# Kernel tuning notes

Hardware: AMD Instinct MI355X
Metric: run time of the kernel (lower is better)

## Reference

```python
import jax, jax.numpy as jnp
import numpy as np

IOU_THRESHOLD = 0.5
NEGATIVE_RATIO = 3
ALPHA = 1.0
B, A, D, G = 64, 8732, 85, 32  # batch, anchors, 4+81 classes, max gt per image


def cxcywh_to_xyxy(b):
    cx, cy, w, h = b[..., 0], b[..., 1], b[..., 2], b[..., 3]
    return jnp.stack([cx - w / 2, cy - h / 2, cx + w / 2, cy + h / 2], axis=-1)


def box_iou(a, b):
    # a: (G,4) xyxy, b: (A,4) xyxy -> (G,A)
    lt = jnp.maximum(a[:, None, :2], b[None, :, :2])
    rb = jnp.minimum(a[:, None, 2:], b[None, :, 2:])
    wh = jnp.clip(rb - lt, 0.0)
    inter = wh[..., 0] * wh[..., 1]
    area_a = (a[:, 2] - a[:, 0]) * (a[:, 3] - a[:, 1])
    area_b = (b[:, 2] - b[:, 0]) * (b[:, 3] - b[:, 1])
    return inter / (area_a[:, None] + area_b[None, :] - inter)


def encode(gt, anchors):
    g_cxcy = (gt[:, :2] - anchors[:, :2]) / anchors[:, 2:]
    g_wh = jnp.log(gt[:, 2:]) - jnp.log(anchors[:, 2:])
    return jnp.concatenate([g_cxcy, g_wh], axis=-1)


def match_one(gt_box, gt_label, count, anchors):
    # gt_box (G,4) cxcywh, gt_label (G,), count scalar, anchors (A,4) cxcywh
    num_anchors = anchors.shape[0]
    valid = jnp.arange(gt_box.shape[0]) < count
    iou = box_iou(cxcywh_to_xyxy(gt_box), cxcywh_to_xyxy(anchors))  # (G,A)
    iou = jnp.where(valid[:, None], iou, -1.0)
    best_gt_overlap = iou.max(0)
    best_gt_idx = iou.argmax(0)
    over = best_gt_overlap > IOU_THRESHOLD
    loc = jnp.where(over[:, None], encode(gt_box[best_gt_idx], anchors), 0.0)
    cls = jnp.where(over, gt_label[best_gt_idx].astype(jnp.float32) + 1.0, 0.0)
    # force-match: each (valid) gt claims its best anchor, overwriting
    best_prior_idx = iou.argmax(1)  # (G,)
    idx = jnp.where(valid, best_prior_idx, num_anchors)  # dump invalid gt into a scratch row
    loc = jnp.concatenate([loc, jnp.zeros((1, 4), loc.dtype)], 0)
    loc = loc.at[idx].set(encode(gt_box, anchors[best_prior_idx]))[:num_anchors]
    cls = jnp.concatenate([cls, jnp.zeros((1,), cls.dtype)], 0)
    cls = cls.at[idx].set(gt_label.astype(jnp.float32) + 1.0)[:num_anchors]
    return loc, cls


def smooth_l1(d):
    ad = jnp.abs(d)
    return jnp.where(ad < 1.0, 0.5 * d * d, ad - 0.5)


def multibox_loss(pred, anchors, gt_boxes, gt_labels, gt_counts):
    num_anchors = pred.shape[1]
    loc_pred, conf_pred = pred[:, :, :4], pred[:, :, 4:]
    target_loc, target_cls = jax.vmap(match_one, in_axes=(0, 0, 0, None))(
        gt_boxes, gt_labels, gt_counts, anchors)  # (B,A,4), (B,A)
    pos = target_cls > 0  # (B,A)
    posf = pos.astype(pred.dtype)
    n_pos = posf.sum(1)  # (B,) guaranteed > 0 since every image has >=1 gt
    # localization: per-element smooth-L1 on positives, normalized per image
    loc_l = smooth_l1(loc_pred - target_loc) * posf[:, :, None]
    loc_loss = jnp.sum(loc_l / n_pos[:, None, None])
    # classification CE per anchor
    logp = jax.nn.log_softmax(conf_pred, axis=-1)  # (B,A,C)
    cls_ce = -jnp.take_along_axis(logp, target_cls.astype(jnp.int32)[:, :, None], axis=-1)[..., 0]
    pos_loss = jnp.sum(cls_ce * posf / n_pos[:, None])
    # hard negative mining (double-sort rank trick, no grad through selection)
    num_neg = jnp.minimum(NEGATIVE_RATIO * pos.sum(1), num_anchors - 1)  # (B,) int
    all_neg = jax.lax.stop_gradient(jnp.where(pos, 0.0, cls_ce))
    order = jnp.argsort(-all_neg, axis=1)
    rank = jnp.argsort(order, axis=1)
    neg_mask = (rank < num_neg[:, None]).astype(pred.dtype)
    neg_ce = -logp[:, :, 0]  # CE against background class 0
    neg_loss = jnp.sum(neg_ce * neg_mask / n_pos[:, None])
    return ALPHA * loc_loss + pos_loss + neg_loss


def setup_inputs() -> dict:
    key = jax.random.key(0)
    k1, k2, k3, k4, k5, k6, k7 = jax.random.split(key, 7)
    pred = jax.random.normal(k1, (B, A, D), dtype=jnp.float32)
    anchors = jnp.concatenate([
        jax.random.uniform(k2, (A, 2), minval=0.0, maxval=1.0),
        jax.random.uniform(k3, (A, 2), minval=0.05, maxval=0.5)], axis=-1)
    gt_boxes = jnp.concatenate([
        jax.random.uniform(k4, (B, G, 2), minval=0.0, maxval=1.0),
        jax.random.uniform(k5, (B, G, 2), minval=0.05, maxval=0.6)], axis=-1)
    gt_labels = jax.random.randint(k6, (B, G), 0, 80)
    gt_counts = jax.random.randint(k7, (B,), 1, G + 1)
    return {"pred": pred, "anchors": anchors, "gt_boxes": gt_boxes,
            "gt_labels": gt_labels, "gt_counts": gt_counts}


def reference(pred, anchors, gt_boxes, gt_labels, gt_counts):
    return multibox_loss(pred, anchors, gt_boxes, gt_labels, gt_counts)
```

## Files before the change

### kernel.cpp

```cpp
#include <hip/hip_runtime.h>
#include <math.h>

#define BB 64
#define AA 8732
#define DD 85
#define GG 32
#define CC 81
#define TILE 64
#define RPB 4
#define NTB 35
#define NAB 35


typedef __attribute__((address_space(3))) unsigned int lds_u32;
typedef const __attribute__((address_space(1))) unsigned int glb_u32;

__device__ __forceinline__ float smoothl1(float d) {
  float ad = fabsf(d);
  return ad < 1.0f ? 0.5f * d * d : ad - 0.5f;
}

__device__ __forceinline__ float frcp(float x) {
  return __builtin_amdgcn_rcpf(x);
}

__global__ __launch_bounds__(256) void k_match(
    const float* __restrict__ anchors, const float* __restrict__ gt_boxes,
    const int* __restrict__ gt_counts, int* __restrict__ match,
    int* __restrict__ bestp, int* __restrict__ n_pos, int* __restrict__ done_sel)
{
  const int b = blockIdx.y;
  const int count = gt_counts[b];
  __shared__ float gx0[GG], gy0[GG], gx1[GG], gy1[GG], gar[GG];
  __shared__ float wv[4];
  __shared__ int wi[4];

  if (blockIdx.x < NAB) {
    if (blockIdx.x == 0 && threadIdx.x == 0) {
      n_pos[b] = 0;
      if (b == 0) *done_sel = 0;
    }
    if (threadIdx.x < GG) {
      float4 gb = reinterpret_cast<const float4*>(gt_boxes)[b * GG + threadIdx.x];
      float x0 = gb.x - gb.z * 0.5f, y0 = gb.y - gb.w * 0.5f;
      float x1 = gb.x + gb.z * 0.5f, y1 = gb.y + gb.w * 0.5f;
      gx0[threadIdx.x] = x0; gy0[threadIdx.x] = y0;
      gx1[threadIdx.x] = x1; gy1[threadIdx.x] = y1;
      gar[threadIdx.x] = (x1 - x0) * (y1 - y0);
    }
    __syncthreads();
    const int a = blockIdx.x * 256 + threadIdx.x;
    if (a < AA) {
      float4 an = reinterpret_cast<const float4*>(anchors)[a];
      float ax0 = an.x - an.z * 0.5f, ay0 = an.y - an.w * 0.5f;
      float ax1 = an.x + an.z * 0.5f, ay1 = an.y + an.w * 0.5f;
      float aar = (ax1 - ax0) * (ay1 - ay0);
      float best = -1.0f; int bi = 0;
      for (int g = 0; g < count; ++g) {
        float iw = fmaxf(fminf(gx1[g], ax1) - fmaxf(gx0[g], ax0), 0.0f);
        float ih = fmaxf(fminf(gy1[g], ay1) - fmaxf(gy0[g], ay0), 0.0f);
        float inter = iw * ih;
        float iou = inter * frcp(gar[g] + aar - inter);
        if (iou > best) { best = iou; bi = g; }
      }
      match[b * AA + a] = (best > 0.5f) ? bi : -1;
    }
  } else {
    const int g = blockIdx.x - NAB;
    if (g < count) {
      float4 gb = reinterpret_cast<const float4*>(gt_boxes)[b * GG + g];
      const float gx0s = gb.x - gb.z * 0.5f, gy0s = gb.y - gb.w * 0.5f;
      const float gx1s = gb.x + gb.z * 0.5f, gy1s = gb.y + gb.w * 0.5f;
      const float gars = (gx1s - gx0s) * (gy1s - gy0s);

      float bv = -2.0f; int bi = AA;
      for (int a = threadIdx.x; a < AA; a += 256) {
        float4 an = reinterpret_cast<const float4*>(anchors)[a];
        float ax0 = an.x - an.z * 0.5f, ay0 = an.y - an.w * 0.5f;
        float ax1 = an.x + an.z * 0.5f, ay1 = an.y + an.w * 0.5f;
        float aar = (ax1 - ax0) * (ay1 - ay0);
        float iw = fmaxf(fminf(gx1s, ax1) - fmaxf(gx0s, ax0), 0.0f);
        float ih = fmaxf(fminf(gy1s, ay1) - fmaxf(gy0s, ay0), 0.0f);
        float inter = iw * ih;
        float iou = inter * frcp(gars + aar - inter);
        if (iou > bv || (iou == bv && a < bi)) { bv = iou; bi = a; }
      }
      #pragma unroll
      for (int m = 1; m < 64; m <<= 1) {
        float ov = __shfl_xor(bv, m);
        int   oi = __shfl_xor(bi, m);
        if (ov > bv || (ov == bv && oi < bi)) { bv = ov; bi = oi; }
      }
      if ((threadIdx.x & 63) == 0) { wv[threadIdx.x >> 6] = bv; wi[threadIdx.x >> 6] = bi; }
      __syncthreads();
      if (threadIdx.x == 0) {
        float fv = wv[0]; int fi = wi[0];
        #pragma unroll
        for (int w = 1; w < 4; ++w)
          if (wv[w] > fv || (wv[w] == fv && wi[w] < fi)) { fv = wv[w]; fi = wi[w]; }
        bestp[b * GG + g] = fi;
      }
    }
  }
}

__global__ __launch_bounds__(256) void k_loss(
    const float* __restrict__ pred, const float* __restrict__ anchors,
    const float* __restrict__ gt_boxes, const int* __restrict__ gt_labels,
    const int* __restrict__ gt_counts, const int* __restrict__ match,
    const int* __restrict__ bestp, float* __restrict__ all_neg,
    float* __restrict__ partials, int* __restrict__ n_pos)
{
  const int b = blockIdx.y;
  const int abase = blockIdx.x * RPB * TILE;
  const int tid = threadIdx.x;
  __shared__ int ovr[RPB * TILE];
  __shared__ float4 sgb[GG];
  __shared__ int slab[GG];
  __shared__ float wsum[4];
  __shared__ int wcnt[4];

  const int cnt = gt_counts[b];
  if (tid < GG) {
    sgb[tid] = reinterpret_cast<const float4*>(gt_boxes)[b * GG + tid];
    slab[tid] = gt_labels[b * GG + tid];
  }
  ovr[tid] = -1;
  __syncthreads();
  if (tid < GG && tid < cnt) {
    int p = bestp[b * GG + tid];
    int rel = p - abase;
    if (rel >= 0 && rel < RPB * TILE) atomicMax(&ovr[rel], tid);
  }
  __syncthreads();

  const int r = tid >> 2;
  const int sub = tid & 3;
  float acc = 0.0f;
  int poscnt = 0;

  for (int i = 0; i < RPB; ++i) {
    const int a0 = abase + i * TILE;
    if (a0 >= AA) break;
    const int a = a0 + r;
    if (a < AA) {
      const float* base = pred + ((size_t)b * AA + a) * DD;
      float4 s0 = *(const float4*)(base + (sub)      * 4);
      float4 s1 = *(const float4*)(base + (sub + 4)  * 4);
      float4 s2 = *(const float4*)(base + (sub + 8)  * 4);
      float4 s3 = *(const float4*)(base + (sub + 12) * 4);
      float4 s4 = *(const float4*)(base + (sub + 16) * 4);
      float4 s5f = make_float4(0.f, 0.f, 0.f, 0.f);
      float  s5x = 0.0f;
      if (sub == 0) s5f = *(const float4*)(base + 80);
      if (sub == 1) s5x = base[84];

      int m = match[b * AA + a];
      { int o = ovr[a - abase]; if (o >= 0) m = o; }
      const int tgt = (m >= 0) ? slab[m] + 1 : 0;

      const int cb = 4 * sub - 4;
      float mx = -INFINITY, xt = -INFINITY;
      #define SCAN(v, ccb)                                                   \
        { mx = fmaxf(fmaxf(fmaxf(mx, (v).x), (v).y), fmaxf((v).z, (v).w));   \
          if ((ccb) + 0 == tgt) xt = (v).x;                                  \
          if ((ccb) + 1 == tgt) xt = (v).y;                                  \
          if ((ccb) + 2 == tgt) xt = (v).z;                                  \
          if ((ccb) + 3 == tgt) xt = (v).w; }
      if (sub > 0) SCAN(s0, cb);
      SCAN(s1, cb + 16); SCAN(s2, cb + 32); SCAN(s3, cb + 48); SCAN(s4, cb + 64);
      if (sub == 0) SCAN(s5f, 76);
      if (sub == 1) { mx = fmaxf(mx, s5x); if (tgt == 80) xt = s5x; }
      #undef SCAN
      #pragma unroll
      for (int msk = 1; msk <= 2; msk <<= 1)
        mx = fmaxf(mx, __shfl_xor(mx, msk));

      float s = 0.0f;
      #define ESUM(v) s += __expf((v).x - mx) + __expf((v).y - mx) +          \
                           __expf((v).z - mx) + __expf((v).w - mx);
      if (sub > 0) ESUM(s0);
      ESUM(s1); ESUM(s2); ESUM(s3); ESUM(s4);
      if (sub == 0) ESUM(s5f);
      if (sub == 1) s += __expf(s5x - mx);
      #undef ESUM
      #pragma unroll
      for (int msk = 1; msk <= 2; msk <<= 1) {
        s  += __shfl_xor(s, msk);
        xt  = fmaxf(xt, __shfl_xor(xt, msk));
      }
      const float lse = mx + __logf(s);
      const float ce = lse - xt;

      if (sub == 0) {
        if (m >= 0) {
          poscnt += 1;
          float4 an = reinterpret_cast<const float4*>(anchors)[a];
          float4 gb = sgb[m];
          float tx = (gb.x - an.x) / an.z;
          float ty = (gb.y - an.y) / an.w;
          float tw = __logf(gb.z) - __logf(an.z);
          float th = __logf(gb.w) - __logf(an.w);
          acc += smoothl1(s0.x - tx) + smoothl1(s0.y - ty)
               + smoothl1(s0.z - tw) + smoothl1(s0.w - th) + ce;
          all_neg[b * AA + a] = 0.0f;
        } else {
          all_neg[b * AA + a] = fmaxf(ce, 0.0f);
        }
      }
    }
  }

  #pragma unroll
  for (int msk = 1; msk < 64; msk <<= 1) {
    acc    += __shfl_xor(acc, msk);
    poscnt += __shfl_xor(poscnt, msk);
  }
  if ((tid & 63) == 0) {
    wsum[tid >> 6] = acc;
    wcnt[tid >> 6] = poscnt;
  }
  __syncthreads();
  if (tid == 0) {
    partials[b * NTB + blockIdx.x] = (wsum[0] + wsum[1]) + (wsum[2] + wsum[3]);
    int c = wcnt[0] + wcnt[1] + wcnt[2] + wcnt[3];
    if (c) atomicAdd(&n_pos[b], c);
  }
}

__global__ __launch_bounds__(1024) void k_select(
    const float* __restrict__ all_neg, const float* __restrict__ partials,
    const int* __restrict__ n_pos, float* __restrict__ batch_total,
    int* __restrict__ done_sel, float* __restrict__ out)
{
  const int b = blockIdx.x;
  const int tid = threadIdx.x;
  __shared__ unsigned u[AA];
  __shared__ int hist16[16][257];
  __shared__ int hist[256];
  __shared__ unsigned sh_pref;
  __shared__ int sh_k;
  __shared__ int sflag;
  __shared__ float wf[16];
  __shared__ int wc[16];

  {
    const float* srcg = all_neg + (size_t)b * AA;
    #pragma unroll
    for (int j = 0; j < 3; ++j) {
      int c = j * 1024 + tid;
      if (c < 2183)
        __builtin_amdgcn_global_load_lds(
            (glb_u32*)(srcg + c * 4), (lds_u32*)((float*)u + c * 4), 16, 0, 0);
    }
  }

  float ps = 0.0f;
  if (tid < 64) {
    float pv = (tid < NTB) ? partials[b * NTB + tid] : 0.0f;
    #pragma unroll
    for (int m = 1; m < 64; m <<= 1) pv += __shfl_xor(pv, m);
    ps = pv;
  }
  __syncthreads();

  const int np = n_pos[b];
  const int K = min(3 * np, AA - 1);
  const int wvid = tid >> 6;

  unsigned prefix = 0;
  int kk = K;
  for (int shift = 24; shift >= 0; shift -= 8) {
    int* hflat = &hist16[0][0];
    for (int i = tid; i < 16 * 257; i += 1024) hflat[i] = 0;
    __syncthreads();
    const unsigned hmask = (shift == 24) ? 0u : (0xFFFFFFFFu << (shift + 8));
    for (int i = tid; i < AA; i += 1024) {
      unsigned x = u[i];
      if ((x & hmask) == prefix)
        atomicAdd(&hist16[wvid][(x >> shift) & 255], 1);
    }
    __syncthreads();
    if (tid < 256) {
      int s = 0;
      #pragma unroll
      for (int h = 0; h < 16; ++h) s += hist16[h][tid];
      hist[tid] = s;
    }
    __syncthreads();
    if (tid < 64) {
      int h0 = hist[4 * tid], h1 = hist[4 * tid + 1];
      int h2 = hist[4 * tid + 2], h3 = hist[4 * tid + 3];
      int lsum = h0 + h1 + h2 + h3;
      int suf = lsum;
      #pragma unroll
      for (int off = 1; off < 64; off <<= 1) {
        int o = __shfl_down(suf, off);
        suf += (tid + off < 64) ? o : 0;
      }
      int after = suf - lsum;
      int s3 = h3 + after, s2 = h2 + s3, s1 = h1 + s2, s0 = h0 + s1;
      if (s0 >= kk && s1 < kk)    { sh_pref = prefix | ((unsigned)(4*tid+0) << shift); sh_k = kk - s1; }
      if (s1 >= kk && s2 < kk)    { sh_pref = prefix | ((unsigned)(4*tid+1) << shift); sh_k = kk - s2; }
      if (s2 >= kk && s3 < kk)    { sh_pref = prefix | ((unsigned)(4*tid+2) << shift); sh_k = kk - s3; }
      if (s3 >= kk && after < kk) { sh_pref = prefix | ((unsigned)(4*tid+3) << shift); sh_k = kk - after; }
    }
    __syncthreads();
    prefix = sh_pref;
    kk = sh_k;
    __syncthreads();
  }
  const float tstar = __uint_as_float(prefix);

  float ssum = 0.0f; int cgt = 0;
  for (int i = tid; i < AA; i += 1024) {
    float x = __uint_as_float(u[i]);
    if (x > tstar) { ssum += x; cgt += 1; }
  }
  #pragma unroll
  for (int m = 1; m < 64; m <<= 1) {
    ssum += __shfl_xor(ssum, m);
    cgt  += __shfl_xor(cgt, m);
  }
  if ((tid & 63) == 0) { wf[wvid] = ssum; wc[wvid] = cgt; }
  __syncthreads();
  if (tid == 0) {
    float S = 0.0f; int Cg = 0;
    #pragma unroll
    for (int w = 0; w < 16; ++w) { S += wf[w]; Cg += wc[w]; }
    float neg_sum = S + (float)(K - Cg) * tstar;
    batch_total[b] = (ps + neg_sum) / (float)np;
    __threadfence();
    int old = atomicAdd(done_sel, 1);
    sflag = (old == BB - 1) ? 1 : 0;
  }
  __syncthreads();

  if (sflag) {
    __threadfence();
    if (tid < 64) {
      float v = batch_total[tid];
      #pragma unroll
      for (int m = 1; m < 64; m <<= 1) v += __shfl_xor(v, m);
      if (tid == 0) out[0] = v;
    }
  }
}

extern "C" void kernel_launch(void* const* d_in, const int* in_sizes, int n_in,
                              void* d_out, int out_size, void* d_ws, size_t ws_size,
                              hipStream_t stream) {
  (void)in_sizes; (void)n_in; (void)out_size; (void)ws_size;
  const float* pred      = (const float*)d_in[0];
  const float* anchors   = (const float*)d_in[1];
  const float* gt_boxes  = (const float*)d_in[2];
  const int*   gt_labels = (const int*)d_in[3];
  const int*   gt_counts = (const int*)d_in[4];

  char* ws = (char*)d_ws;
  int*   match       = (int*)(ws + 0);
  float* all_neg     = (float*)(ws + 2235392);
  float* partials    = (float*)(ws + 4470784);
  float* batch_total = (float*)(ws + 4479744);
  int*   bestp       = (int*)(ws + 4480000);
  int*   n_pos       = (int*)(ws + 4488192);
  int*   done_sel    = (int*)(ws + 4488448);
  float* out = (float*)d_out;

  hipLaunchKernelGGL(k_match, dim3(NAB + GG, BB), dim3(256), 0, stream,
                     anchors, gt_boxes, gt_counts, match, bestp, n_pos, done_sel);
  hipLaunchKernelGGL(k_loss, dim3(NTB, BB), dim3(256), 0, stream,
                     pred, anchors, gt_boxes, gt_labels, gt_counts, match, bestp,
                     all_neg, partials, n_pos);
  hipLaunchKernelGGL(k_select, dim3(BB), dim3(1024), 0, stream,
                     all_neg, partials, n_pos, batch_total, done_sel, out);
}
```

Baseline: 85.41 us.

## Fuse matching into loss kernel and apply force-match corrections in select

New measurement: 89.84 us. 5.2% more time.

```diff
diff --git a/kernel.cpp b/kernel.cpp
--- a/kernel.cpp
+++ b/kernel.cpp
@@ -8,8 +8,8 @@
 #define CC 81
 #define TILE 64
 #define RPB 4
-#define NTB 35
-#define NAB 35
+#define NLB 35
+#define NSB GG
 
 
 typedef __attribute__((address_space(3))) unsigned int lds_u32;
@@ -24,222 +24,202 @@
   return __builtin_amdgcn_rcpf(x);
 }
 
-__global__ __launch_bounds__(256) void k_match(
-    const float* __restrict__ anchors, const float* __restrict__ gt_boxes,
-    const int* __restrict__ gt_counts, int* __restrict__ match,
-    int* __restrict__ bestp, int* __restrict__ n_pos, int* __restrict__ done_sel)
+__global__ __launch_bounds__(256) void k_fused(
+    const float* __restrict__ pred, const float* __restrict__ anchors,
+    const float* __restrict__ gt_boxes, const int* __restrict__ gt_labels,
+    const int* __restrict__ gt_counts, float* __restrict__ all_neg,
+    float* __restrict__ partials, int* __restrict__ poscnts,
+    int* __restrict__ bestp, unsigned* __restrict__ epoch)
 {
   const int b = blockIdx.y;
-  const int count = gt_counts[b];
-  __shared__ float gx0[GG], gy0[GG], gx1[GG], gy1[GG], gar[GG];
-  __shared__ float wv[4];
-  __shared__ int wi[4];
-
-  if (blockIdx.x < NAB) {
-    if (blockIdx.x == 0 && threadIdx.x == 0) {
-      n_pos[b] = 0;
-      if (b == 0) *done_sel = 0;
-    }
-    if (threadIdx.x < GG) {
-      float4 gb = reinterpret_cast<const float4*>(gt_boxes)[b * GG + threadIdx.x];
+  const int tid = threadIdx.x;
+  const int cnt = gt_counts[b];
+
+  __shared__ float sgx0[GG], sgy0[GG], sgx1[GG], sgy1[GG], sgar[GG];
+  __shared__ float4 sgb[GG];
+  __shared__ int slab[GG];
+  __shared__ float wsum[4];
+  __shared__ int wcnt[4];
+
+  if (blockIdx.x < NLB) {
+    if (blockIdx.x == 0 && b == 0 && tid == 0) *epoch = 0u;
+    if (tid < GG) {
+      float4 gb = reinterpret_cast<const float4*>(gt_boxes)[b * GG + tid];
+      sgb[tid] = gb;
       float x0 = gb.x - gb.z * 0.5f, y0 = gb.y - gb.w * 0.5f;
       float x1 = gb.x + gb.z * 0.5f, y1 = gb.y + gb.w * 0.5f;
-      gx0[threadIdx.x] = x0; gy0[threadIdx.x] = y0;
-      gx1[threadIdx.x] = x1; gy1[threadIdx.x] = y1;
-      gar[threadIdx.x] = (x1 - x0) * (y1 - y0);
-    }
-    __syncthreads();
-    const int a = blockIdx.x * 256 + threadIdx.x;
-    if (a < AA) {
+      sgx0[tid] = x0; sgy0[tid] = y0; sgx1[tid] = x1; sgy1[tid] = y1;
+      sgar[tid] = (x1 - x0) * (y1 - y0);
+      slab[tid] = gt_labels[b * GG + tid];
+    }
+    __syncthreads();
+
+    const int abase = blockIdx.x * RPB * TILE;
+    const int r = tid >> 2;
+    const int sub = tid & 3;
+    float acc = 0.0f;
+    int poscnt = 0;
+
+    for (int i = 0; i < RPB; ++i) {
+      const int a0 = abase + i * TILE;
+      if (a0 >= AA) break;
+      const int a = a0 + r;
+      if (a < AA) {
+        const float* base = pred + ((size_t)b * AA + a) * DD;
+        float4 s0 = *(const float4*)(base + (sub)      * 4);
+        float4 s1 = *(const float4*)(base + (sub + 4)  * 4);
+        float4 s2 = *(const float4*)(base + (sub + 8)  * 4);
+        float4 s3 = *(const float4*)(base + (sub + 12) * 4);
+        float4 s4 = *(const float4*)(base + (sub + 16) * 4);
+        float4 s5f = make_float4(0.f, 0.f, 0.f, 0.f);
+        float  s5x = 0.0f;
+        if (sub == 0) s5f = *(const float4*)(base + 80);
+        if (sub == 1) s5x = base[84];
+        float4 an = reinterpret_cast<const float4*>(anchors)[a];
+
+        float ax0 = an.x - an.z * 0.5f, ay0 = an.y - an.w * 0.5f;
+        float ax1 = an.x + an.z * 0.5f, ay1 = an.y + an.w * 0.5f;
+        float aar = (ax1 - ax0) * (ay1 - ay0);
+        float bv = -1.0f; int bg = 0;
+        for (int g = sub; g < cnt; g += 4) {
+          float iw = fmaxf(fminf(sgx1[g], ax1) - fmaxf(sgx0[g], ax0), 0.0f);
+          float ih = fmaxf(fminf(sgy1[g], ay1) - fmaxf(sgy0[g], ay0), 0.0f);
+          float inter = iw * ih;
+          float iou = inter * frcp(sgar[g] + aar - inter);
+          if (iou > bv) { bv = iou; bg = g; }
+        }
+        #pragma unroll
+        for (int msk = 1; msk <= 2; msk <<= 1) {
+          float ov = __shfl_xor(bv, msk);
+          int   og = __shfl_xor(bg, msk);
+          if (ov > bv || (ov == bv && og < bg)) { bv = ov; bg = og; }
+        }
+        const int m = (bv > 0.5f) ? bg : -1;
+        const int tgt = (m >= 0) ? slab[m] + 1 : 0;
+
+        const int cb = 4 * sub - 4;
+        float mx = -INFINITY, xt = -INFINITY;
+        #define SCAN(v, ccb)                                                 \
+          { mx = fmaxf(fmaxf(fmaxf(mx, (v).x), (v).y), fmaxf((v).z, (v).w)); \
+            if ((ccb) + 0 == tgt) xt = (v).x;                                \
+            if ((ccb) + 1 == tgt) xt = (v).y;                                \
+            if ((ccb) + 2 == tgt) xt = (v).z;                                \
+            if ((ccb) + 3 == tgt) xt = (v).w; }
+        if (sub > 0) SCAN(s0, cb);
+        SCAN(s1, cb + 16); SCAN(s2, cb + 32); SCAN(s3, cb + 48); SCAN(s4, cb + 64);
+        if (sub == 0) SCAN(s5f, 76);
+        if (sub == 1) { mx = fmaxf(mx, s5x); if (tgt == 80) xt = s5x; }
+        #undef SCAN
+        #pragma unroll
+        for (int msk = 1; msk <= 2; msk <<= 1)
+          mx = fmaxf(mx, __shfl_xor(mx, msk));
+
+        float s = 0.0f;
+        #define ESUM(v) s += __expf((v).x - mx) + __expf((v).y - mx) +        \
+                             __expf((v).z - mx) + __expf((v).w - mx);
+        if (sub > 0) ESUM(s0);
+        ESUM(s1); ESUM(s2); ESUM(s3); ESUM(s4);
+        if (sub == 0) ESUM(s5f);
+        if (sub == 1) s += __expf(s5x - mx);
+        #undef ESUM
+        #pragma unroll
+        for (int msk = 1; msk <= 2; msk <<= 1) {
+          s  += __shfl_xor(s, msk);
+          xt  = fmaxf(xt, __shfl_xor(xt, msk));
+        }
+        const float lse = mx + __logf(s);
+        const float ce = lse - xt;
+
+        if (sub == 0) {
+          if (m >= 0) {
+            poscnt += 1;
+            float4 gb = sgb[m];
+            float tx = (gb.x - an.x) / an.z;
+            float ty = (gb.y - an.y) / an.w;
+            float tw = __logf(gb.z) - __logf(an.z);
+            float th = __logf(gb.w) - __logf(an.w);
+            acc += smoothl1(s0.x - tx) + smoothl1(s0.y - ty)
+                 + smoothl1(s0.z - tw) + smoothl1(s0.w - th) + ce;
+            all_neg[b * AA + a] = 0.0f;
+          } else {
+            all_neg[b * AA + a] = fmaxf(ce, 0.0f);
+          }
+        }
+      }
+    }
+
+    #pragma unroll
+    for (int msk = 1; msk < 64; msk <<= 1) {
+      acc    += __shfl_xor(acc, msk);
+      poscnt += __shfl_xor(poscnt, msk);
+    }
+    if ((tid & 63) == 0) { wsum[tid >> 6] = acc; wcnt[tid >> 6] = poscnt; }
+    __syncthreads();
+    if (tid == 0) {
+      partials[b * NLB + blockIdx.x] = (wsum[0] + wsum[1]) + (wsum[2] + wsum[3]);
+      poscnts[b * NLB + blockIdx.x] = wcnt[0] + wcnt[1] + wcnt[2] + wcnt[3];
+    }
+  } else {
+    const int g = blockIdx.x - NLB;
+    if (g >= cnt) return;
+
+    float4 gb = reinterpret_cast<const float4*>(gt_boxes)[b * GG + g];
+    const float gx0s = gb.x - gb.z * 0.5f, gy0s = gb.y - gb.w * 0.5f;
+    const float gx1s = gb.x + gb.z * 0.5f, gy1s = gb.y + gb.w * 0.5f;
+    const float gars = (gx1s - gx0s) * (gy1s - gy0s);
+
+    float bv = -2.0f; int bi = AA;
+    for (int a = tid; a < AA; a += 256) {
       float4 an = reinterpret_cast<const float4*>(anchors)[a];
       float ax0 = an.x - an.z * 0.5f, ay0 = an.y - an.w * 0.5f;
       float ax1 = an.x + an.z * 0.5f, ay1 = an.y + an.w * 0.5f;
       float aar = (ax1 - ax0) * (ay1 - ay0);
-      float best = -1.0f; int bi = 0;
-      for (int g = 0; g < count; ++g) {
-        float iw = fmaxf(fminf(gx1[g], ax1) - fmaxf(gx0[g], ax0), 0.0f);
-        float ih = fmaxf(fminf(gy1[g], ay1) - fmaxf(gy0[g], ay0), 0.0f);
-        float inter = iw * ih;
-        float iou = inter * frcp(gar[g] + aar - inter);
-        if (iou > best) { best = iou; bi = g; }
-      }
-      match[b * AA + a] = (best > 0.5f) ? bi : -1;
-    }
-  } else {
-    const int g = blockIdx.x - NAB;
-    if (g < count) {
-      float4 gb = reinterpret_cast<const float4*>(gt_boxes)[b * GG + g];
-      const float gx0s = gb.x - gb.z * 0.5f, gy0s = gb.y - gb.w * 0.5f;
-      const float gx1s = gb.x + gb.z * 0.5f, gy1s = gb.y + gb.w * 0.5f;
-      const float gars = (gx1s - gx0s) * (gy1s - gy0s);
-
-      float bv = -2.0f; int bi = AA;
-      for (int a = threadIdx.x; a < AA; a += 256) {
-        float4 an = reinterpret_cast<const float4*>(anchors)[a];
-        float ax0 = an.x - an.z * 0.5f, ay0 = an.y - an.w * 0.5f;
-        float ax1 = an.x + an.z * 0.5f, ay1 = an.y + an.w * 0.5f;
-        float aar = (ax1 - ax0) * (ay1 - ay0);
-        float iw = fmaxf(fminf(gx1s, ax1) - fmaxf(gx0s, ax0), 0.0f);
-        float ih = fmaxf(fminf(gy1s, ay1) - fmaxf(gy0s, ay0), 0.0f);
-        float inter = iw * ih;
-        float iou = inter * frcp(gars + aar - inter);
-        if (iou > bv || (iou == bv && a < bi)) { bv = iou; bi = a; }
-      }
+      float iw = fmaxf(fminf(gx1s, ax1) - fmaxf(gx0s, ax0), 0.0f);
+      float ih = fmaxf(fminf(gy1s, ay1) - fmaxf(gy0s, ay0), 0.0f);
+      float inter = iw * ih;
+      float iou = inter * frcp(gars + aar - inter);
+      if (iou > bv || (iou == bv && a < bi)) { bv = iou; bi = a; }
+    }
+    #pragma unroll
+    for (int m = 1; m < 64; m <<= 1) {
+      float ov = __shfl_xor(bv, m);
+      int   oi = __shfl_xor(bi, m);
+      if (ov > bv || (ov == bv && oi < bi)) { bv = ov; bi = oi; }
+    }
+    if ((tid & 63) == 0) { wsum[tid >> 6] = bv; wcnt[tid >> 6] = bi; }
+    __syncthreads();
+    if (tid == 0) {
+      float fv = wsum[0]; int fi = wcnt[0];
       #pragma unroll
-      for (int m = 1; m < 64; m <<= 1) {
-        float ov = __shfl_xor(bv, m);
-        int   oi = __shfl_xor(bi, m);
-        if (ov > bv || (ov == bv && oi < bi)) { bv = ov; bi = oi; }
-      }
-      if ((threadIdx.x & 63) == 0) { wv[threadIdx.x >> 6] = bv; wi[threadIdx.x >> 6] = bi; }
-      __syncthreads();
-      if (threadIdx.x == 0) {
-        float fv = wv[0]; int fi = wi[0];
-        #pragma unroll
-        for (int w = 1; w < 4; ++w)
-          if (wv[w] > fv || (wv[w] == fv && wi[w] < fi)) { fv = wv[w]; fi = wi[w]; }
-        bestp[b * GG + g] = fi;
-      }
+      for (int w = 1; w < 4; ++w)
+        if (wsum[w] > fv || (wsum[w] == fv && wcnt[w] < fi)) { fv = wsum[w]; fi = wcnt[w]; }
+      bestp[b * GG + g] = fi;
     }
   }
 }
 
-__global__ __launch_bounds__(256) void k_loss(
+__global__ __launch_bounds__(1024) void k_select(
     const float* __restrict__ pred, const float* __restrict__ anchors,
     const float* __restrict__ gt_boxes, const int* __restrict__ gt_labels,
-    const int* __restrict__ gt_counts, const int* __restrict__ match,
-    const int* __restrict__ bestp, float* __restrict__ all_neg,
-    float* __restrict__ partials, int* __restrict__ n_pos)
-{
-  const int b = blockIdx.y;
-  const int abase = blockIdx.x * RPB * TILE;
-  const int tid = threadIdx.x;
-  __shared__ int ovr[RPB * TILE];
-  __shared__ float4 sgb[GG];
-  __shared__ int slab[GG];
-  __shared__ float wsum[4];
-  __shared__ int wcnt[4];
-
-  const int cnt = gt_counts[b];
-  if (tid < GG) {
-    sgb[tid] = reinterpret_cast<const float4*>(gt_boxes)[b * GG + tid];
-    slab[tid] = gt_labels[b * GG + tid];
-  }
-  ovr[tid] = -1;
-  __syncthreads();
-  if (tid < GG && tid < cnt) {
-    int p = bestp[b * GG + tid];
-    int rel = p - abase;
-    if (rel >= 0 && rel < RPB * TILE) atomicMax(&ovr[rel], tid);
-  }
-  __syncthreads();
-
-  const int r = tid >> 2;
-  const int sub = tid & 3;
-  float acc = 0.0f;
-  int poscnt = 0;
-
-  for (int i = 0; i < RPB; ++i) {
-    const int a0 = abase + i * TILE;
-    if (a0 >= AA) break;
-    const int a = a0 + r;
-    if (a < AA) {
-      const float* base = pred + ((size_t)b * AA + a) * DD;
-      float4 s0 = *(const float4*)(base + (sub)      * 4);
-      float4 s1 = *(const float4*)(base + (sub + 4)  * 4);
-      float4 s2 = *(const float4*)(base + (sub + 8)  * 4);
-      float4 s3 = *(const float4*)(base + (sub + 12) * 4);
-      float4 s4 = *(const float4*)(base + (sub + 16) * 4);
-      float4 s5f = make_float4(0.f, 0.f, 0.f, 0.f);
-      float  s5x = 0.0f;
-      if (sub == 0) s5f = *(const float4*)(base + 80);
-      if (sub == 1) s5x = base[84];
-
-      int m = match[b * AA + a];
-      { int o = ovr[a - abase]; if (o >= 0) m = o; }
-      const int tgt = (m >= 0) ? slab[m] + 1 : 0;
-
-      const int cb = 4 * sub - 4;
-      float mx = -INFINITY, xt = -INFINITY;
-      #define SCAN(v, ccb)                                                   \
-        { mx = fmaxf(fmaxf(fmaxf(mx, (v).x), (v).y), fmaxf((v).z, (v).w));   \
-          if ((ccb) + 0 == tgt) xt = (v).x;                                  \
-          if ((ccb) + 1 == tgt) xt = (v).y;                                  \
-          if ((ccb) + 2 == tgt) xt = (v).z;                                  \
-          if ((ccb) + 3 == tgt) xt = (v).w; }
-      if (sub > 0) SCAN(s0, cb);
-      SCAN(s1, cb + 16); SCAN(s2, cb + 32); SCAN(s3, cb + 48); SCAN(s4, cb + 64);
-      if (sub == 0) SCAN(s5f, 76);
-      if (sub == 1) { mx = fmaxf(mx, s5x); if (tgt == 80) xt = s5x; }
-      #undef SCAN
-      #pragma unroll
-      for (int msk = 1; msk <= 2; msk <<= 1)
-        mx = fmaxf(mx, __shfl_xor(mx, msk));
-
-      float s = 0.0f;
-      #define ESUM(v) s += __expf((v).x - mx) + __expf((v).y - mx) +          \
-                           __expf((v).z - mx) + __expf((v).w - mx);
-      if (sub > 0) ESUM(s0);
-      ESUM(s1); ESUM(s2); ESUM(s3); ESUM(s4);
-      if (sub == 0) ESUM(s5f);
-      if (sub == 1) s += __expf(s5x - mx);
-      #undef ESUM
-      #pragma unroll
-      for (int msk = 1; msk <= 2; msk <<= 1) {
-        s  += __shfl_xor(s, msk);
-        xt  = fmaxf(xt, __shfl_xor(xt, msk));
-      }
-      const float lse = mx + __logf(s);
-      const float ce = lse - xt;
-
-      if (sub == 0) {
-        if (m >= 0) {
-          poscnt += 1;
-          float4 an = reinterpret_cast<const float4*>(anchors)[a];
-          float4 gb = sgb[m];
-          float tx = (gb.x - an.x) / an.z;
-          float ty = (gb.y - an.y) / an.w;
-          float tw = __logf(gb.z) - __logf(an.z);
-          float th = __logf(gb.w) - __logf(an.w);
-          acc += smoothl1(s0.x - tx) + smoothl1(s0.y - ty)
-               + smoothl1(s0.z - tw) + smoothl1(s0.w - th) + ce;
-          all_neg[b * AA + a] = 0.0f;
-        } else {
-          all_neg[b * AA + a] = fmaxf(ce, 0.0f);
-        }
-      }
-    }
-  }
-
-  #pragma unroll
-  for (int msk = 1; msk < 64; msk <<= 1) {
-    acc    += __shfl_xor(acc, msk);
-    poscnt += __shfl_xor(poscnt, msk);
-  }
-  if ((tid & 63) == 0) {
-    wsum[tid >> 6] = acc;
-    wcnt[tid >> 6] = poscnt;
-  }
-  __syncthreads();
-  if (tid == 0) {
-    partials[b * NTB + blockIdx.x] = (wsum[0] + wsum[1]) + (wsum[2] + wsum[3]);
-    int c = wcnt[0] + wcnt[1] + wcnt[2] + wcnt[3];
-    if (c) atomicAdd(&n_pos[b], c);
-  }
-}
-
-__global__ __launch_bounds__(1024) void k_select(
-    const float* __restrict__ all_neg, const float* __restrict__ partials,
-    const int* __restrict__ n_pos, float* __restrict__ batch_total,
-    int* __restrict__ done_sel, float* __restrict__ out)
+    const int* __restrict__ gt_counts, const float* __restrict__ all_neg,
+    const float* __restrict__ partials, const int* __restrict__ poscnts,
+    const int* __restrict__ bestp, float* __restrict__ batch_total,
+    unsigned* __restrict__ epoch, float* __restrict__ out)
 {
   const int b = blockIdx.x;
   const int tid = threadIdx.x;
   __shared__ unsigned u[AA];
   __shared__ int hist16[16][257];
   __shared__ int hist[256];
+  __shared__ float sgx0[GG], sgy0[GG], sgx1[GG], sgy1[GG], sgar[GG];
+  __shared__ float4 sgb[GG];
+  __shared__ int slab[GG];
+  __shared__ float sdelta[GG];
+  __shared__ int sdnp[GG];
   __shared__ unsigned sh_pref;
   __shared__ int sh_k;
+  __shared__ int sh_np;
+  __shared__ float sh_base;
   __shared__ int sflag;
   __shared__ float wf[16];
   __shared__ int wc[16];
@@ -254,22 +234,89 @@
             (glb_u32*)(srcg + c * 4), (lds_u32*)((float*)u + c * 4), 16, 0, 0);
     }
   }
-
-  float ps = 0.0f;
+  if (tid < GG) {
+    float4 gb = reinterpret_cast<const float4*>(gt_boxes)[b * GG + tid];
+    sgb[tid] = gb;
+    float x0 = gb.x - gb.z * 0.5f, y0 = gb.y - gb.w * 0.5f;
+    float x1 = gb.x + gb.z * 0.5f, y1 = gb.y + gb.w * 0.5f;
+    sgx0[tid] = x0; sgy0[tid] = y0; sgx1[tid] = x1; sgy1[tid] = y1;
+    sgar[tid] = (x1 - x0) * (y1 - y0);
+    slab[tid] = gt_labels[b * GG + tid];
+    sdelta[tid] = 0.0f; sdnp[tid] = 0;
+  }
+
+  float ps = 0.0f; int pc = 0;
   if (tid < 64) {
-    float pv = (tid < NTB) ? partials[b * NTB + tid] : 0.0f;
+    float pv = (tid < NLB) ? partials[b * NLB + tid] : 0.0f;
+    int   cv = (tid < NLB) ? poscnts[b * NLB + tid] : 0;
     #pragma unroll
-    for (int m = 1; m < 64; m <<= 1) pv += __shfl_xor(pv, m);
-    ps = pv;
+    for (int m = 1; m < 64; m <<= 1) { pv += __shfl_xor(pv, m); cv += __shfl_xor(cv, m); }
+    ps = pv; pc = cv;
   }
   __syncthreads();
 
-  const int np = n_pos[b];
-  const int K = min(3 * np, AA - 1);
+  const int cnt = gt_counts[b];
+  if (tid < cnt) {
+    const int g = tid;
+    const int p = bestp[b * GG + g];
+    bool last = true;
+    for (int g2 = g + 1; g2 < cnt; ++g2)
+      if (bestp[b * GG + g2] == p) last = false;
+    if (last) {
+      const float* row = pred + ((size_t)b * AA + p) * DD;
+      float mx = -INFINITY;
+      for (int c = 0; c < CC; ++c) mx = fmaxf(mx, row[4 + c]);
+      float s = 0.0f;
+      for (int c = 0; c < CC; ++c) s += __expf(row[4 + c] - mx);
+      const float lse = mx + __logf(s);
+      float4 an = reinterpret_cast<const float4*>(anchors)[p];
+      float ax0 = an.x - an.z * 0.5f, ay0 = an.y - an.w * 0.5f;
+      float ax1 = an.x + an.z * 0.5f, ay1 = an.y + an.w * 0.5f;
+      float aar = (ax1 - ax0) * (ay1 - ay0);
+      float bv = -1.0f; int bg = 0;
+      for (int g2 = 0; g2 < cnt; ++g2) {
+        float iw = fmaxf(fminf(sgx1[g2], ax1) - fmaxf(sgx0[g2], ax0), 0.0f);
+        float ih = fmaxf(fminf(sgy1[g2], ay1) - fmaxf(sgy0[g2], ay0), 0.0f);
+        float inter = iw * ih;
+        float iou = inter * frcp(sgar[g2] + aar - inter);
+        if (iou > bv) { bv = iou; bg = g2; }
+      }
+      const int m_old = (bv > 0.5f) ? bg : -1;
+
+      auto posterm = [&](int m) -> float {
+        const int tgt = slab[m] + 1;
+        float ce = lse - row[4 + tgt];
+        float4 gb = sgb[m];
+        float tx = (gb.x - an.x) / an.z;
+        float ty = (gb.y - an.y) / an.w;
+        float tw = __logf(gb.z) - __logf(an.z);
+        float th = __logf(gb.w) - __logf(an.w);
+        return smoothl1(row[0] - tx) + smoothl1(row[1] - ty)
+             + smoothl1(row[2] - tw) + smoothl1(row[3] - th) + ce;
+      };
+      float delta = posterm(g) - ((m_old >= 0) ? posterm(m_old) : 0.0f);
+      sdelta[g] = delta;
+      sdnp[g] = (m_old < 0) ? 1 : 0;
+      u[p] = 0u;
+    }
+  }
+  __syncthreads();
+
+  if (tid == 0) {
+    float dl = 0.0f; int dn = 0;
+    for (int g = 0; g < cnt; ++g) { dl += sdelta[g]; dn += sdnp[g]; }
+    const int npf = pc + dn;
+    sh_np = npf;
+    sh_base = ps + dl;
+    sh_k = min(3 * npf, AA - 1);
+  }
+  __syncthreads();
+
+  const int np = sh_np;
   const int wvid = tid >> 6;
 
   unsigned prefix = 0;
-  int kk = K;
+  int kk = sh_k;
   for (int shift = 24; shift >= 0; shift -= 8) {
     int* hflat = &hist16[0][0];
     for (int i = tid; i < 16 * 257; i += 1024) hflat[i] = 0;
@@ -311,6 +358,7 @@
     __syncthreads();
   }
   const float tstar = __uint_as_float(prefix);
+  const int K = min(3 * np, AA - 1);
 
   float ssum = 0.0f; int cgt = 0;
   for (int i = tid; i < AA; i += 1024) {
@@ -329,10 +377,10 @@
     #pragma unroll
     for (int w = 0; w < 16; ++w) { S += wf[w]; Cg += wc[w]; }
     float neg_sum = S + (float)(K - Cg) * tstar;
-    batch_total[b] = (ps + neg_sum) / (float)np;
+    batch_total[b] = (sh_base + neg_sum) / (float)np;
     __threadfence();
-    int old = atomicAdd(done_sel, 1);
-    sflag = (old == BB - 1) ? 1 : 0;
+    unsigned old = atomicAdd(epoch, 1u);
+    sflag = (old == (unsigned)(BB - 1)) ? 1 : 0;
   }
   __syncthreads();
 
@@ -358,20 +406,18 @@
   const int*   gt_counts = (const int*)d_in[4];
 
   char* ws = (char*)d_ws;
-  int*   match       = (int*)(ws + 0);
-  float* all_neg     = (float*)(ws + 2235392);
-  float* partials    = (float*)(ws + 4470784);
-  float* batch_total = (float*)(ws + 4479744);
-  int*   bestp       = (int*)(ws + 4480000);
-  int*   n_pos       = (int*)(ws + 4488192);
-  int*   done_sel    = (int*)(ws + 4488448);
+  float*    all_neg     = (float*)(ws + 0);
+  float*    partials    = (float*)(ws + 2235392);
+  int*      poscnts     = (int*)(ws + 2244352);
+  float*    batch_total = (float*)(ws + 2253312);
+  int*      bestp       = (int*)(ws + 2253568);
+  unsigned* epoch       = (unsigned*)(ws + 2261760);
   float* out = (float*)d_out;
 
-  hipLaunchKernelGGL(k_match, dim3(NAB + GG, BB), dim3(256), 0, stream,
-                     anchors, gt_boxes, gt_counts, match, bestp, n_pos, done_sel);
-  hipLaunchKernelGGL(k_loss, dim3(NTB, BB), dim3(256), 0, stream,
-                     pred, anchors, gt_boxes, gt_labels, gt_counts, match, bestp,
-                     all_neg, partials, n_pos);
+  hipLaunchKernelGGL(k_fused, dim3(NLB + NSB, BB), dim3(256), 0, stream,
+                     pred, anchors, gt_boxes, gt_labels, gt_counts,
+                     all_neg, partials, poscnts, bestp, epoch);
   hipLaunchKernelGGL(k_select, dim3(BB), dim3(1024), 0, stream,
-                     all_neg, partials, n_pos, batch_total, done_sel, out);
+                     pred, anchors, gt_boxes, gt_labels, gt_counts,
+                     all_neg, partials, poscnts, bestp, batch_total, epoch, out);
 }
```

## Fuse per-anchor IoU matching into loss kernel, drop match buffer

Applied to the files above, without the earlier changes.

New measurement: 80.83 us, median of 2. -5.4%, faster.

```diff
diff --git a/kernel.cpp b/kernel.cpp
--- a/kernel.cpp
+++ b/kernel.cpp
@@ -8,8 +8,7 @@
 #define CC 81
 #define TILE 64
 #define RPB 4
-#define NTB 35
-#define NAB 35
+#define NLB 35
 
 
 typedef __attribute__((address_space(3))) unsigned int lds_u32;
@@ -24,113 +23,112 @@
   return __builtin_amdgcn_rcpf(x);
 }
 
-__global__ __launch_bounds__(256) void k_match(
+__global__ __launch_bounds__(256) void k_matchB(
     const float* __restrict__ anchors, const float* __restrict__ gt_boxes,
-    const int* __restrict__ gt_counts, int* __restrict__ match,
-    int* __restrict__ bestp, int* __restrict__ n_pos, int* __restrict__ done_sel)
+    const int* __restrict__ gt_counts, int* __restrict__ bestp,
+    int* __restrict__ n_pos, int* __restrict__ done_sel)
+{
+  const int g = blockIdx.x;
+  const int b = blockIdx.y;
+  if (g == 0 && threadIdx.x == 0) {
+    n_pos[b] = 0;
+    if (b == 0) *done_sel = 0;
+  }
+  if (g >= gt_counts[b]) return;
+
+  __shared__ float wv[4];
+  __shared__ int wi[4];
+
+  float4 gb = reinterpret_cast<const float4*>(gt_boxes)[b * GG + g];
+  const float gx0s = gb.x - gb.z * 0.5f, gy0s = gb.y - gb.w * 0.5f;
+  const float gx1s = gb.x + gb.z * 0.5f, gy1s = gb.y + gb.w * 0.5f;
+  const float gars = (gx1s - gx0s) * (gy1s - gy0s);
+
+  float bv = -2.0f; int bi = AA;
+  for (int a = threadIdx.x; a < AA; a += 256) {
+    float4 an = reinterpret_cast<const float4*>(anchors)[a];
+    float ax0 = an.x - an.z * 0.5f, ay0 = an.y - an.w * 0.5f;
+    float ax1 = an.x + an.z * 0.5f, ay1 = an.y + an.w * 0.5f;
+    float aar = (ax1 - ax0) * (ay1 - ay0);
+    float iw = fmaxf(fminf(gx1s, ax1) - fmaxf(gx0s, ax0), 0.0f);
+    float ih = fmaxf(fminf(gy1s, ay1) - fmaxf(gy0s, ay0), 0.0f);
+    float inter = iw * ih;
+    float iou = inter * frcp(gars + aar - inter);
+    if (iou > bv || (iou == bv && a < bi)) { bv = iou; bi = a; }
+  }
+  #pragma unroll
+  for (int m = 1; m < 64; m <<= 1) {
+    float ov = __shfl_xor(bv, m);
+    int   oi = __shfl_xor(bi, m);
+    if (ov > bv || (ov == bv && oi < bi)) { bv = ov; bi = oi; }
+  }
+  if ((threadIdx.x & 63) == 0) { wv[threadIdx.x >> 6] = bv; wi[threadIdx.x >> 6] = bi; }
+  __syncthreads();
+  if (threadIdx.x == 0) {
+    float fv = wv[0]; int fi = wi[0];
+    #pragma unroll
+    for (int w = 1; w < 4; ++w)
+      if (wv[w] > fv || (wv[w] == fv && wi[w] < fi)) { fv = wv[w]; fi = wi[w]; }
+    bestp[b * GG + g] = fi;
+  }
+}
+
+__global__ __launch_bounds__(256) void k_loss(
+    const float* __restrict__ pred, const float* __restrict__ anchors,
+    const float* __restrict__ gt_boxes, const int* __restrict__ gt_labels,
+    const int* __restrict__ gt_counts, const int* __restrict__ bestp,
+    float* __restrict__ all_neg, float* __restrict__ partials,
+    int* __restrict__ n_pos)
 {
   const int b = blockIdx.y;
-  const int count = gt_counts[b];
-  __shared__ float gx0[GG], gy0[GG], gx1[GG], gy1[GG], gar[GG];
-  __shared__ float wv[4];
-  __shared__ int wi[4];
-
-  if (blockIdx.x < NAB) {
-    if (blockIdx.x == 0 && threadIdx.x == 0) {
-      n_pos[b] = 0;
-      if (b == 0) *done_sel = 0;
-    }
-    if (threadIdx.x < GG) {
-      float4 gb = reinterpret_cast<const float4*>(gt_boxes)[b * GG + threadIdx.x];
-      float x0 = gb.x - gb.z * 0.5f, y0 = gb.y - gb.w * 0.5f;
-      float x1 = gb.x + gb.z * 0.5f, y1 = gb.y + gb.w * 0.5f;
-      gx0[threadIdx.x] = x0; gy0[threadIdx.x] = y0;
-      gx1[threadIdx.x] = x1; gy1[threadIdx.x] = y1;
-      gar[threadIdx.x] = (x1 - x0) * (y1 - y0);
-    }
-    __syncthreads();
-    const int a = blockIdx.x * 256 + threadIdx.x;
+  const int tid = threadIdx.x;
+  const int abase = blockIdx.x * RPB * TILE;
+  const int cnt = gt_counts[b];
+
+  __shared__ float sgx0[GG], sgy0[GG], sgx1[GG], sgy1[GG], sgar[GG];
+  __shared__ float4 sgb[GG];
+  __shared__ int slab[GG];
+  __shared__ int smatch[RPB * TILE];
+  __shared__ int ovrg[RPB * TILE];
+  __shared__ float wsum[4];
+  __shared__ int wcnt[4];
+
+  if (tid < GG) {
+    float4 gb = reinterpret_cast<const float4*>(gt_boxes)[b * GG + tid];
+    sgb[tid] = gb;
+    float x0 = gb.x - gb.z * 0.5f, y0 = gb.y - gb.w * 0.5f;
+    float x1 = gb.x + gb.z * 0.5f, y1 = gb.y + gb.w * 0.5f;
+    sgx0[tid] = x0; sgy0[tid] = y0; sgx1[tid] = x1; sgy1[tid] = y1;
+    sgar[tid] = (x1 - x0) * (y1 - y0);
+    slab[tid] = gt_labels[b * GG + tid];
+  }
+  ovrg[tid] = -1;
+  __syncthreads();
+
+  {
+    const int a = abase + tid;
+    int mres = -1;
     if (a < AA) {
       float4 an = reinterpret_cast<const float4*>(anchors)[a];
       float ax0 = an.x - an.z * 0.5f, ay0 = an.y - an.w * 0.5f;
       float ax1 = an.x + an.z * 0.5f, ay1 = an.y + an.w * 0.5f;
       float aar = (ax1 - ax0) * (ay1 - ay0);
       float best = -1.0f; int bi = 0;
-      for (int g = 0; g < count; ++g) {
-        float iw = fmaxf(fminf(gx1[g], ax1) - fmaxf(gx0[g], ax0), 0.0f);
-        float ih = fmaxf(fminf(gy1[g], ay1) - fmaxf(gy0[g], ay0), 0.0f);
+      for (int g = 0; g < cnt; ++g) {
+        float iw = fmaxf(fminf(sgx1[g], ax1) - fmaxf(sgx0[g], ax0), 0.0f);
+        float ih = fmaxf(fminf(sgy1[g], ay1) - fmaxf(sgy0[g], ay0), 0.0f);
         float inter = iw * ih;
-        float iou = inter * frcp(gar[g] + aar - inter);
+        float iou = inter * frcp(sgar[g] + aar - inter);
         if (iou > best) { best = iou; bi = g; }
       }
-      match[b * AA + a] = (best > 0.5f) ? bi : -1;
-    }
-  } else {
-    const int g = blockIdx.x - NAB;
-    if (g < count) {
-      float4 gb = reinterpret_cast<const float4*>(gt_boxes)[b * GG + g];
-      const float gx0s = gb.x - gb.z * 0.5f, gy0s = gb.y - gb.w * 0.5f;
-      const float gx1s = gb.x + gb.z * 0.5f, gy1s = gb.y + gb.w * 0.5f;
-      const float gars = (gx1s - gx0s) * (gy1s - gy0s);
-
-      float bv = -2.0f; int bi = AA;
-      for (int a = threadIdx.x; a < AA; a += 256) {
-        float4 an = reinterpret_cast<const float4*>(anchors)[a];
-        float ax0 = an.x - an.z * 0.5f, ay0 = an.y - an.w * 0.5f;
-        float ax1 = an.x + an.z * 0.5f, ay1 = an.y + an.w * 0.5f;
-        float aar = (ax1 - ax0) * (ay1 - ay0);
-        float iw = fmaxf(fminf(gx1s, ax1) - fmaxf(gx0s, ax0), 0.0f);
-        float ih = fmaxf(fminf(gy1s, ay1) - fmaxf(gy0s, ay0), 0.0f);
-        float inter = iw * ih;
-        float iou = inter * frcp(gars + aar - inter);
-        if (iou > bv || (iou == bv && a < bi)) { bv = iou; bi = a; }
-      }
-      #pragma unroll
-      for (int m = 1; m < 64; m <<= 1) {
-        float ov = __shfl_xor(bv, m);
-        int   oi = __shfl_xor(bi, m);
-        if (ov > bv || (ov == bv && oi < bi)) { bv = ov; bi = oi; }
-      }
-      if ((threadIdx.x & 63) == 0) { wv[threadIdx.x >> 6] = bv; wi[threadIdx.x >> 6] = bi; }
-      __syncthreads();
-      if (threadIdx.x == 0) {
-        float fv = wv[0]; int fi = wi[0];
-        #pragma unroll
-        for (int w = 1; w < 4; ++w)
-          if (wv[w] > fv || (wv[w] == fv && wi[w] < fi)) { fv = wv[w]; fi = wi[w]; }
-        bestp[b * GG + g] = fi;
-      }
-    }
-  }
-}
-
-__global__ __launch_bounds__(256) void k_loss(
-    const float* __restrict__ pred, const float* __restrict__ anchors,
-    const float* __restrict__ gt_boxes, const int* __restrict__ gt_labels,
-    const int* __restrict__ gt_counts, const int* __restrict__ match,
-    const int* __restrict__ bestp, float* __restrict__ all_neg,
-    float* __restrict__ partials, int* __restrict__ n_pos)
-{
-  const int b = blockIdx.y;
-  const int abase = blockIdx.x * RPB * TILE;
-  const int tid = threadIdx.x;
-  __shared__ int ovr[RPB * TILE];
-  __shared__ float4 sgb[GG];
-  __shared__ int slab[GG];
-  __shared__ float wsum[4];
-  __shared__ int wcnt[4];
-
-  const int cnt = gt_counts[b];
-  if (tid < GG) {
-    sgb[tid] = reinterpret_cast<const float4*>(gt_boxes)[b * GG + tid];
-    slab[tid] = gt_labels[b * GG + tid];
-  }
-  ovr[tid] = -1;
-  __syncthreads();
+      mres = (best > 0.5f) ? bi : -1;
+    }
+    smatch[tid] = mres;
+  }
   if (tid < GG && tid < cnt) {
     int p = bestp[b * GG + tid];
     int rel = p - abase;
-    if (rel >= 0 && rel < RPB * TILE) atomicMax(&ovr[rel], tid);
+    if (rel >= 0 && rel < RPB * TILE) atomicMax(&ovrg[rel], tid);
   }
   __syncthreads();
 
@@ -155,8 +153,8 @@
       if (sub == 0) s5f = *(const float4*)(base + 80);
       if (sub == 1) s5x = base[84];
 
-      int m = match[b * AA + a];
-      { int o = ovr[a - abase]; if (o >= 0) m = o; }
+      int m;
+      { int o = ovrg[a - abase]; m = (o >= 0) ? o : smatch[a - abase]; }
       const int tgt = (m >= 0) ? slab[m] + 1 : 0;
 
       const int cb = 4 * sub - 4;
@@ -222,7 +220,7 @@
   }
   __syncthreads();
   if (tid == 0) {
-    partials[b * NTB + blockIdx.x] = (wsum[0] + wsum[1]) + (wsum[2] + wsum[3]);
+    partials[b * NLB + blockIdx.x] = (wsum[0] + wsum[1]) + (wsum[2] + wsum[3]);
     int c = wcnt[0] + wcnt[1] + wcnt[2] + wcnt[3];
     if (c) atomicAdd(&n_pos[b], c);
   }
@@ -257,7 +255,7 @@
 
   float ps = 0.0f;
   if (tid < 64) {
-    float pv = (tid < NTB) ? partials[b * NTB + tid] : 0.0f;
+    float pv = (tid < NLB) ? partials[b * NLB + tid] : 0.0f;
     #pragma unroll
     for (int m = 1; m < 64; m <<= 1) pv += __shfl_xor(pv, m);
     ps = pv;
@@ -358,19 +356,18 @@
   const int*   gt_counts = (const int*)d_in[4];
 
   char* ws = (char*)d_ws;
-  int*   match       = (int*)(ws + 0);
-  float* all_neg     = (float*)(ws + 2235392);
-  float* partials    = (float*)(ws + 4470784);
-  float* batch_total = (float*)(ws + 4479744);
-  int*   bestp       = (int*)(ws + 4480000);
-  int*   n_pos       = (int*)(ws + 4488192);
-  int*   done_sel    = (int*)(ws + 4488448);
+  float* all_neg     = (float*)(ws + 0);
+  float* partials    = (float*)(ws + 2235392);
+  float* batch_total = (float*)(ws + 2244352);
+  int*   bestp       = (int*)(ws + 2244608);
+  int*   n_pos       = (int*)(ws + 2252800);
+  int*   done_sel    = (int*)(ws + 2253056);
   float* out = (float*)d_out;
 
-  hipLaunchKernelGGL(k_match, dim3(NAB + GG, BB), dim3(256), 0, stream,
-                     anchors, gt_boxes, gt_counts, match, bestp, n_pos, done_sel);
-  hipLaunchKernelGGL(k_loss, dim3(NTB, BB), dim3(256), 0, stream,
-                     pred, anchors, gt_boxes, gt_labels, gt_counts, match, bestp,
+  hipLaunchKernelGGL(k_matchB, dim3(GG, BB), dim3(256), 0, stream,
+                     anchors, gt_boxes, gt_counts, bestp, n_pos, done_sel);
+  hipLaunchKernelGGL(k_loss, dim3(NLB, BB), dim3(256), 0, stream,
+                     pred, anchors, gt_boxes, gt_labels, gt_counts, bestp,
                      all_neg, partials, n_pos);
   hipLaunchKernelGGL(k_select, dim3(BB), dim3(1024), 0, stream,
                      all_neg, partials, n_pos, batch_total, done_sel, out);
```
